# Performance work log

Hardware: AMD Instinct MI355X
Metric: run time of the kernel (lower is better)

## Reference

```python
import jax, jax.numpy as jnp
import numpy as np


def setup_inputs() -> dict:
    key = jax.random.key(0)
    k1, k2, k3 = jax.random.split(key, 3)
    B, T, D, U = 64, 1024, 256, 256
    inputs = jax.random.normal(k1, (B, T, D), dtype=jnp.float32)
    W_xh = jax.random.normal(k2, (D, U), dtype=jnp.float32) * (1.0 / np.sqrt(D))
    W_hh = jax.random.normal(k3, (U, U), dtype=jnp.float32) * (1.0 / np.sqrt(U))
    b_h = jnp.zeros((U,), dtype=jnp.float32)
    return {"inputs": inputs, "W_xh": W_xh, "W_hh": W_hh, "b_h": b_h}


def reference(inputs, W_xh, W_hh, b_h):
    # inputs: [B, T, D]. Precompute input projection (same math as per-step matmul),
    # then scan the sequential recurrence: h_t = tanh(xW_t + h_{t-1} @ W_hh + b).
    B = inputs.shape[0]
    U = W_hh.shape[0]
    xW = jnp.einsum('btd,du->btu', inputs, W_xh) + b_h  # [B, T, U]
    h0 = jnp.zeros((B, U), dtype=inputs.dtype)

    def step(h, xw_t):
        h_new = jnp.tanh(xw_t + h @ W_hh)
        return h_new, h_new

    _, hs = jax.lax.scan(step, h0, jnp.swapaxes(xW, 0, 1))  # hs: [T, B, U]
    return jnp.swapaxes(hs, 0, 1)  # [B, T, U] (return_sequences=True)
```

## Files before the change

kernel.cpp:

```cpp
#include <hip/hip_runtime.h>
#include <math.h>

#define B_ 64
#define T_ 1024
#define D_ 256
#define U_ 256

typedef __fp16   hf2_t __attribute__((ext_vector_type(2)));
typedef _Float16 f16x8 __attribute__((ext_vector_type(8)));
typedef float    f32x4 __attribute__((ext_vector_type(4)));

__global__ __launch_bounds__(256, 2)
void proj_gemm_mfma(const float* __restrict__ A,
                    const float* __restrict__ Bm,
                    const float* __restrict__ bias,
                    float* __restrict__ C) {
    __shared__ __align__(16) _Float16 As[64 * 256];

    const int tid  = (int)threadIdx.x;
    const int lane = tid & 63;
    const int w    = tid >> 6;
    const int g    = lane >> 4;
    const int c    = lane & 15;
    const int m0   = (int)blockIdx.x * 64;
    const int n0   = (int)blockIdx.y * 64 + w * 16;

    f16x8 bf[8];
    #pragma unroll
    for (int kt = 0; kt < 8; ++kt) {
        f16x8 v;
        #pragma unroll
        for (int j = 0; j < 8; ++j)
            v[j] = (_Float16)Bm[(kt * 32 + g * 8 + j) * U_ + n0 + c];
        bf[kt] = v;
    }

    #pragma unroll
    for (int i = 0; i < 8; ++i) {
        const int chunk = tid + 256 * i;
        const int row   = chunk >> 5;
        const int k8    = (chunk & 31) * 8;
        const float4 f0 = *(const float4*)&A[(size_t)(m0 + row) * D_ + k8];
        const float4 f1 = *(const float4*)&A[(size_t)(m0 + row) * D_ + k8 + 4];
        union { hf2_t p[4]; f16x8 v; } u;
        u.p[0] = __builtin_amdgcn_cvt_pkrtz(f0.x, f0.y);
        u.p[1] = __builtin_amdgcn_cvt_pkrtz(f0.z, f0.w);
        u.p[2] = __builtin_amdgcn_cvt_pkrtz(f1.x, f1.y);
        u.p[3] = __builtin_amdgcn_cvt_pkrtz(f1.z, f1.w);
        *(f16x8*)((char*)As + row * 512 + ((k8 * 2) ^ ((row & 7) << 4))) = u.v;
    }
    __syncthreads();

    const int swz   = (lane & 7) << 4;
    const int vbase = c * 512 + ((g * 16) ^ swz);

    f32x4 acc[4];
    #pragma unroll
    for (int mt = 0; mt < 4; ++mt) acc[mt] = f32x4{0.f, 0.f, 0.f, 0.f};

    #pragma unroll
    for (int kt = 0; kt < 8; ++kt) {
        const char* ap = (const char*)As + (vbase ^ (kt * 64));
        #pragma unroll
        for (int mt = 0; mt < 4; ++mt) {
            f16x8 a = *(const f16x8*)(ap + mt * 8192);
            acc[mt] = __builtin_amdgcn_mfma_f32_16x16x32_f16(a, bf[kt],
                                                             acc[mt], 0, 0, 0);
        }
    }

    const float bb = bias[n0 + c];
    #pragma unroll
    for (int mt = 0; mt < 4; ++mt) {
        #pragma unroll
        for (int r = 0; r < 4; ++r) {
            const int row = m0 + mt * 16 + g * 4 + r;
            C[(size_t)row * U_ + n0 + c] = acc[mt][r] + bb;
        }
    }
}

__device__ __forceinline__ float fast_tanh2(float x) {
    float e = __expf(2.0f * x);
    return 1.0f - 2.0f * __builtin_amdgcn_rcpf(e + 1.0f);
}

#define CH_  16
#define NCH_ (T_ / CH_)
#define NT2_ 512

__global__ __launch_bounds__(NT2_) __attribute__((amdgpu_waves_per_eu(2, 2)))
void rnn_scan(const float* __restrict__ W_hh,
              float* __restrict__ out) {
    const int b    = (int)blockIdx.x;
    const int tid  = (int)threadIdx.x;
    const int w    = tid >> 6;
    const int lane = tid & 63;
    const int g    = lane >> 4;
    const int c    = lane & 15;
    const int n0   = w * 32;

    __shared__ float buf[2][CH_][U_];
    __shared__ __align__(16) _Float16 hl[2][U_];

    f16x8 bf[8][2];
    #pragma unroll
    for (int kt = 0; kt < 8; ++kt) {
        #pragma unroll
        for (int nt = 0; nt < 2; ++nt) {
            f16x8 v;
            #pragma unroll
            for (int j = 0; j < 8; ++j)
                v[j] = (_Float16)W_hh[(size_t)(kt * 32 + g * 8 + j) * U_
                                      + (n0 + nt * 16 + c)];
            bf[kt][nt] = v;
        }
    }

    if (tid < 128) ((float*)&hl[0][0])[tid] = 0.f;

    float* gbase = out + (size_t)b * T_ * U_;
    float* bufflat = &buf[0][0][0];

    {
        float4 v0 = *(const float4*)&gbase[8 * tid];
        float4 v1 = *(const float4*)&gbase[8 * tid + 4];
        *(float4*)&bufflat[8 * tid]     = v0;
        *(float4*)&bufflat[8 * tid + 4] = v1;
    }
    __syncthreads();

    float4 p0, p1;
    {
        const float* gsrc = gbase + (size_t)CH_ * U_;
        p0 = *(const float4*)&gsrc[8 * tid];
        p1 = *(const float4*)&gsrc[8 * tid + 4];
    }

    const char* hrd = (const char*)&hl[0][0] + g * 16;
    char*       hwr = (char*)&hl[0][0] + (n0 + c) * 2;

#define STEP(J)                                                               \
    {                                                                         \
        const int RD = ((J) & 1) * 512;                                       \
        const int WR = 512 - RD;                                              \
        const float xw0 = *(const float*)(bufc + (J) * 1024);                 \
        const float xw1 = *(const float*)(bufc + (J) * 1024 + 64);            \
        f32x4 a0 = {0.f, 0.f, 0.f, 0.f};                                      \
        f32x4 a1 = {0.f, 0.f, 0.f, 0.f};                                      \
        _Pragma("unroll") for (int kt = 0; kt < 8; ++kt) {                    \
            f16x8 a = *(const f16x8*)(hrd + RD + 64 * kt);                    \
            a0 = __builtin_amdgcn_mfma_f32_16x16x32_f16(a, bf[kt][0], a0,     \
                                                        0, 0, 0);             \
            a1 = __builtin_amdgcn_mfma_f32_16x16x32_f16(a, bf[kt][1], a1,     \
                                                        0, 0, 0);             \
        }                                                                     \
        const float h0 = fast_tanh2(a0[0] + xw0);                             \
        const float h1 = fast_tanh2(a1[0] + xw1);                             \
        if (g == 0) {                                                         \
            *(float*)(bufc + (J) * 1024)      = h0;                           \
            *(float*)(bufc + (J) * 1024 + 64) = h1;                           \
            *(_Float16*)(hwr + WR)      = (_Float16)h0;                       \
            *(_Float16*)(hwr + WR + 32) = (_Float16)h1;                       \
        }                                                                     \
        asm volatile("s_waitcnt lgkmcnt(0)" ::: "memory");                    \
        __builtin_amdgcn_s_barrier();                                         \
        asm volatile("" ::: "memory");                                        \
    }

    int cur = 0;
    for (int ch = 0; ch < NCH_; ++ch) {
        char* bufc = (char*)bufflat + cur * 16384 + (n0 + c) * 4;

        STEP(0)  STEP(1)  STEP(2)  STEP(3)
        STEP(4)  STEP(5)  STEP(6)  STEP(7)
        STEP(8)  STEP(9)  STEP(10) STEP(11)
        STEP(12) STEP(13) STEP(14) STEP(15)

        float4 d0 = *(const float4*)&bufflat[cur * 4096 + 8 * tid];
        float4 d1 = *(const float4*)&bufflat[cur * 4096 + 8 * tid + 4];

        if (ch + 1 < NCH_) {
            *(float4*)&bufflat[(1 - cur) * 4096 + 8 * tid]     = p0;
            *(float4*)&bufflat[(1 - cur) * 4096 + 8 * tid + 4] = p1;
        }

        asm volatile("s_waitcnt lgkmcnt(0)" ::: "memory");
        __builtin_amdgcn_s_barrier();
        asm volatile("" ::: "memory");

        {
            float* gdst = gbase + (size_t)ch * CH_ * U_;
            *(float4*)&gdst[8 * tid]     = d0;
            *(float4*)&gdst[8 * tid + 4] = d1;
        }
        if (ch + 2 < NCH_) {
            const float* gsrc = gbase + (size_t)(ch + 2) * CH_ * U_;
            p0 = *(const float4*)&gsrc[8 * tid];
            p1 = *(const float4*)&gsrc[8 * tid + 4];
        }
        cur ^= 1;
    }
#undef STEP
}

extern "C" void kernel_launch(void* const* d_in, const int* in_sizes, int n_in,
                              void* d_out, int out_size, void* d_ws, size_t ws_size,
                              hipStream_t stream) {
    const float* inputs = (const float*)d_in[0];
    const float* W_xh   = (const float*)d_in[1];
    const float* W_hh   = (const float*)d_in[2];
    const float* b_h    = (const float*)d_in[3];
    float* out = (float*)d_out;

    const int M = B_ * T_;
    dim3 g1(M / 64, U_ / 64);
    proj_gemm_mfma<<<g1, 256, 0, stream>>>(inputs, W_xh, b_h, out);
    rnn_scan<<<B_, NT2_, 0, stream>>>(W_hh, out);
}
```

Measured before the change: 622.0 us.

## Fuse input projection GEMM into the recurrent scan kernel per chunk

Removes the separate projection GEMM kernel. The scan kernel now loads each 16-timestep chunk of inputs, converts it to fp16 in shared memory, and computes x@W_xh+b with MFMA into the double buffer for the next chunk. This avoids writing xW to global memory and reading it back, and saves one kernel launch. In exchange, the projection work moves onto the serial critical path of only 64 blocks, which adds register pressure (W_xh kept in registers) and an extra barrier per chunk. The h@W_hh reduction is also split into two independent accumulator chains to shorten the dependent MFMA chain.

Result: faster. 580.1 us (-6.7%).

```diff
diff --git a/kernel.cpp b/kernel.cpp
--- a/kernel.cpp
+++ b/kernel.cpp
@@ -10,76 +10,6 @@
 typedef _Float16 f16x8 __attribute__((ext_vector_type(8)));
 typedef float    f32x4 __attribute__((ext_vector_type(4)));
 
-__global__ __launch_bounds__(256, 2)
-void proj_gemm_mfma(const float* __restrict__ A,
-                    const float* __restrict__ Bm,
-                    const float* __restrict__ bias,
-                    float* __restrict__ C) {
-    __shared__ __align__(16) _Float16 As[64 * 256];
-
-    const int tid  = (int)threadIdx.x;
-    const int lane = tid & 63;
-    const int w    = tid >> 6;
-    const int g    = lane >> 4;
-    const int c    = lane & 15;
-    const int m0   = (int)blockIdx.x * 64;
-    const int n0   = (int)blockIdx.y * 64 + w * 16;
-
-    f16x8 bf[8];
-    #pragma unroll
-    for (int kt = 0; kt < 8; ++kt) {
-        f16x8 v;
-        #pragma unroll
-        for (int j = 0; j < 8; ++j)
-            v[j] = (_Float16)Bm[(kt * 32 + g * 8 + j) * U_ + n0 + c];
-        bf[kt] = v;
-    }
-
-    #pragma unroll
-    for (int i = 0; i < 8; ++i) {
-        const int chunk = tid + 256 * i;
-        const int row   = chunk >> 5;
-        const int k8    = (chunk & 31) * 8;
-        const float4 f0 = *(const float4*)&A[(size_t)(m0 + row) * D_ + k8];
-        const float4 f1 = *(const float4*)&A[(size_t)(m0 + row) * D_ + k8 + 4];
-        union { hf2_t p[4]; f16x8 v; } u;
-        u.p[0] = __builtin_amdgcn_cvt_pkrtz(f0.x, f0.y);
-        u.p[1] = __builtin_amdgcn_cvt_pkrtz(f0.z, f0.w);
-        u.p[2] = __builtin_amdgcn_cvt_pkrtz(f1.x, f1.y);
-        u.p[3] = __builtin_amdgcn_cvt_pkrtz(f1.z, f1.w);
-        *(f16x8*)((char*)As + row * 512 + ((k8 * 2) ^ ((row & 7) << 4))) = u.v;
-    }
-    __syncthreads();
-
-    const int swz   = (lane & 7) << 4;
-    const int vbase = c * 512 + ((g * 16) ^ swz);
-
-    f32x4 acc[4];
-    #pragma unroll
-    for (int mt = 0; mt < 4; ++mt) acc[mt] = f32x4{0.f, 0.f, 0.f, 0.f};
-
-    #pragma unroll
-    for (int kt = 0; kt < 8; ++kt) {
-        const char* ap = (const char*)As + (vbase ^ (kt * 64));
-        #pragma unroll
-        for (int mt = 0; mt < 4; ++mt) {
-            f16x8 a = *(const f16x8*)(ap + mt * 8192);
-            acc[mt] = __builtin_amdgcn_mfma_f32_16x16x32_f16(a, bf[kt],
-                                                             acc[mt], 0, 0, 0);
-        }
-    }
-
-    const float bb = bias[n0 + c];
-    #pragma unroll
-    for (int mt = 0; mt < 4; ++mt) {
-        #pragma unroll
-        for (int r = 0; r < 4; ++r) {
-            const int row = m0 + mt * 16 + g * 4 + r;
-            C[(size_t)row * U_ + n0 + c] = acc[mt][r] + bb;
-        }
-    }
-}
-
 __device__ __forceinline__ float fast_tanh2(float x) {
     float e = __expf(2.0f * x);
     return 1.0f - 2.0f * __builtin_amdgcn_rcpf(e + 1.0f);
@@ -90,8 +20,11 @@
 #define NT2_ 512
 
 __global__ __launch_bounds__(NT2_) __attribute__((amdgpu_waves_per_eu(2, 2)))
-void rnn_scan(const float* __restrict__ W_hh,
-              float* __restrict__ out) {
+void rnn_fused(const float* __restrict__ inputs,
+               const float* __restrict__ W_xh,
+               const float* __restrict__ W_hh,
+               const float* __restrict__ b_h,
+               float* __restrict__ out) {
     const int b    = (int)blockIdx.x;
     const int tid  = (int)threadIdx.x;
     const int w    = tid >> 6;
@@ -102,40 +35,86 @@
 
     __shared__ float buf[2][CH_][U_];
     __shared__ __align__(16) _Float16 hl[2][U_];
-
-    f16x8 bf[8][2];
+    __shared__ __align__(16) _Float16 Ax[CH_ * D_];
+
+    f16x8 whh[8][2], wxh[8][2];
     #pragma unroll
     for (int kt = 0; kt < 8; ++kt) {
         #pragma unroll
         for (int nt = 0; nt < 2; ++nt) {
-            f16x8 v;
+            f16x8 vh, vx;
             #pragma unroll
-            for (int j = 0; j < 8; ++j)
-                v[j] = (_Float16)W_hh[(size_t)(kt * 32 + g * 8 + j) * U_
-                                      + (n0 + nt * 16 + c)];
-            bf[kt][nt] = v;
+            for (int j = 0; j < 8; ++j) {
+                const int row = kt * 32 + g * 8 + j;
+                const int col = n0 + nt * 16 + c;
+                vh[j] = (_Float16)W_hh[(size_t)row * U_ + col];
+                vx[j] = (_Float16)W_xh[(size_t)row * U_ + col];
+            }
+            whh[kt][nt] = vh;
+            wxh[kt][nt] = vx;
         }
     }
+    const float bb0 = b_h[n0 + c];
+    const float bb1 = b_h[n0 + 16 + c];
 
     if (tid < 128) ((float*)&hl[0][0])[tid] = 0.f;
 
+    const float* ibase = inputs + (size_t)b * T_ * D_;
     float* gbase = out + (size_t)b * T_ * U_;
     float* bufflat = &buf[0][0][0];
 
+    const int srow = tid >> 5;
+    const int sk8  = (tid & 31) * 8;
+    char* const sdst = (char*)Ax + srow * 512 + ((sk8 * 2) ^ ((srow & 7) << 4));
+
+    const int vbaseA = c * 512 + ((g * 16) ^ ((c & 7) << 4));
+
+#define PACK8(DST, F0, F1)                                                    \
+    {                                                                         \
+        union { hf2_t p[4]; f16x8 v; } u;                                     \
+        u.p[0] = __builtin_amdgcn_cvt_pkrtz((F0).x, (F0).y);                  \
+        u.p[1] = __builtin_amdgcn_cvt_pkrtz((F0).z, (F0).w);                  \
+        u.p[2] = __builtin_amdgcn_cvt_pkrtz((F1).x, (F1).y);                  \
+        u.p[3] = __builtin_amdgcn_cvt_pkrtz((F1).z, (F1).w);                  \
+        *(f16x8*)(DST) = u.v;                                                 \
+    }
+
+#define PROJECT(PB)                                                           \
+    {                                                                         \
+        f32x4 q0 = {0.f,0.f,0.f,0.f}, q1 = {0.f,0.f,0.f,0.f};                 \
+        f32x4 q2 = {0.f,0.f,0.f,0.f}, q3 = {0.f,0.f,0.f,0.f};                 \
+        _Pragma("unroll") for (int kt = 0; kt < 4; ++kt) {                    \
+            f16x8 a = *(const f16x8*)((const char*)Ax + (vbaseA ^ (kt * 64)));\
+            q0 = __builtin_amdgcn_mfma_f32_16x16x32_f16(a, wxh[kt][0], q0, 0, 0, 0); \
+            q1 = __builtin_amdgcn_mfma_f32_16x16x32_f16(a, wxh[kt][1], q1, 0, 0, 0); \
+        }                                                                     \
+        _Pragma("unroll") for (int kt = 4; kt < 8; ++kt) {                    \
+            f16x8 a = *(const f16x8*)((const char*)Ax + (vbaseA ^ (kt * 64)));\
+            q2 = __builtin_amdgcn_mfma_f32_16x16x32_f16(a, wxh[kt][0], q2, 0, 0, 0); \
+            q3 = __builtin_amdgcn_mfma_f32_16x16x32_f16(a, wxh[kt][1], q3, 0, 0, 0); \
+        }                                                                     \
+        _Pragma("unroll") for (int r = 0; r < 4; ++r) {                       \
+            buf[PB][g * 4 + r][n0 + c]      = q0[r] + q2[r] + bb0;            \
+            buf[PB][g * 4 + r][n0 + 16 + c] = q1[r] + q3[r] + bb1;            \
+        }                                                                     \
+    }
+
     {
-        float4 v0 = *(const float4*)&gbase[8 * tid];
-        float4 v1 = *(const float4*)&gbase[8 * tid + 4];
-        *(float4*)&bufflat[8 * tid]     = v0;
-        *(float4*)&bufflat[8 * tid + 4] = v1;
+        float4 f0 = *(const float4*)&ibase[8 * tid];
+        float4 f1 = *(const float4*)&ibase[8 * tid + 4];
+        PACK8(sdst, f0, f1)
     }
     __syncthreads();
-
+    PROJECT(0)
     float4 p0, p1;
     {
-        const float* gsrc = gbase + (size_t)CH_ * U_;
+        const float* gsrc = ibase + (size_t)CH_ * D_;
         p0 = *(const float4*)&gsrc[8 * tid];
         p1 = *(const float4*)&gsrc[8 * tid + 4];
     }
+    asm volatile("s_waitcnt lgkmcnt(0)" ::: "memory");
+    __builtin_amdgcn_s_barrier();
+    asm volatile("" ::: "memory");
 
     const char* hrd = (const char*)&hl[0][0] + g * 16;
     char*       hwr = (char*)&hl[0][0] + (n0 + c) * 2;
@@ -146,17 +125,20 @@
         const int WR = 512 - RD;                                              \
         const float xw0 = *(const float*)(bufc + (J) * 1024);                 \
         const float xw1 = *(const float*)(bufc + (J) * 1024 + 64);            \
-        f32x4 a0 = {0.f, 0.f, 0.f, 0.f};                                      \
-        f32x4 a1 = {0.f, 0.f, 0.f, 0.f};                                      \
-        _Pragma("unroll") for (int kt = 0; kt < 8; ++kt) {                    \
+        f32x4 a0 = {0.f,0.f,0.f,0.f}, a1 = {0.f,0.f,0.f,0.f};                 \
+        f32x4 c0 = {0.f,0.f,0.f,0.f}, c1 = {0.f,0.f,0.f,0.f};                 \
+        _Pragma("unroll") for (int kt = 0; kt < 4; ++kt) {                    \
             f16x8 a = *(const f16x8*)(hrd + RD + 64 * kt);                    \
-            a0 = __builtin_amdgcn_mfma_f32_16x16x32_f16(a, bf[kt][0], a0,     \
-                                                        0, 0, 0);             \
-            a1 = __builtin_amdgcn_mfma_f32_16x16x32_f16(a, bf[kt][1], a1,     \
-                                                        0, 0, 0);             \
-        }                                                                     \
-        const float h0 = fast_tanh2(a0[0] + xw0);                             \
-        const float h1 = fast_tanh2(a1[0] + xw1);                             \
+            a0 = __builtin_amdgcn_mfma_f32_16x16x32_f16(a, whh[kt][0], a0, 0, 0, 0); \
+            a1 = __builtin_amdgcn_mfma_f32_16x16x32_f16(a, whh[kt][1], a1, 0, 0, 0); \
+        }                                                                     \
+        _Pragma("unroll") for (int kt = 4; kt < 8; ++kt) {                    \
+            f16x8 a = *(const f16x8*)(hrd + RD + 64 * kt);                    \
+            c0 = __builtin_amdgcn_mfma_f32_16x16x32_f16(a, whh[kt][0], c0, 0, 0, 0); \
+            c1 = __builtin_amdgcn_mfma_f32_16x16x32_f16(a, whh[kt][1], c1, 0, 0, 0); \
+        }                                                                     \
+        const float h0 = fast_tanh2(a0[0] + c0[0] + xw0);                     \
+        const float h1 = fast_tanh2(a1[0] + c1[0] + xw1);                     \
         if (g == 0) {                                                         \
             *(float*)(bufc + (J) * 1024)      = h0;                           \
             *(float*)(bufc + (J) * 1024 + 64) = h1;                           \
@@ -180,14 +162,13 @@
         float4 d0 = *(const float4*)&bufflat[cur * 4096 + 8 * tid];
         float4 d1 = *(const float4*)&bufflat[cur * 4096 + 8 * tid + 4];
 
-        if (ch + 1 < NCH_) {
-            *(float4*)&bufflat[(1 - cur) * 4096 + 8 * tid]     = p0;
-            *(float4*)&bufflat[(1 - cur) * 4096 + 8 * tid + 4] = p1;
-        }
+        if (ch + 1 < NCH_) PACK8(sdst, p0, p1)
 
         asm volatile("s_waitcnt lgkmcnt(0)" ::: "memory");
         __builtin_amdgcn_s_barrier();
         asm volatile("" ::: "memory");
+
+        if (ch + 1 < NCH_) PROJECT(1 - cur)
 
         {
             float* gdst = gbase + (size_t)ch * CH_ * U_;
@@ -195,13 +176,20 @@
             *(float4*)&gdst[8 * tid + 4] = d1;
         }
         if (ch + 2 < NCH_) {
-            const float* gsrc = gbase + (size_t)(ch + 2) * CH_ * U_;
+            const float* gsrc = ibase + (size_t)(ch + 2) * CH_ * D_;
             p0 = *(const float4*)&gsrc[8 * tid];
             p1 = *(const float4*)&gsrc[8 * tid + 4];
         }
+
+        asm volatile("s_waitcnt lgkmcnt(0)" ::: "memory");
+        __builtin_amdgcn_s_barrier();
+        asm volatile("" ::: "memory");
+
         cur ^= 1;
     }
 #undef STEP
+#undef PROJECT
+#undef PACK8
 }
 
 extern "C" void kernel_launch(void* const* d_in, const int* in_sizes, int n_in,
@@ -213,8 +201,5 @@
     const float* b_h    = (const float*)d_in[3];
     float* out = (float*)d_out;
 
-    const int M = B_ * T_;
-    dim3 g1(M / 64, U_ / 64);
-    proj_gemm_mfma<<<g1, 256, 0, stream>>>(inputs, W_xh, b_h, out);
-    rnn_scan<<<B_, NT2_, 0, stream>>>(W_hh, out);
+    rnn_fused<<<B_, NT2_, 0, stream>>>(inputs, W_xh, W_hh, b_h, out);
 }
```
